# Performance work log

Hardware: AMD Instinct MI355X
Metric: run time of the kernel (lower is better)

## Reference

```python
import jax, jax.numpy as jnp
import numpy as np

B = 32768; E = 9; RANK = 50; K = 2
N_ENT = 40943; N_REL = 22
LOSS_COEF = 0.01; NOISE_EPS = 0.01
EPS = float(np.finfo(np.float64).eps)


def setup_inputs():
    key = jax.random.key(0)
    ks = jax.random.split(key, 12)
    q0 = jax.random.randint(ks[0], (B,), 0, N_ENT)
    q1 = jax.random.randint(ks[1], (B,), 0, N_REL)
    q2 = jax.random.randint(ks[2], (B,), 0, N_ENT)
    queries = jnp.stack([q0, q1, q2], axis=1)
    t2 = jax.random.randint(ks[3], (B,), 0, N_ENT)
    these_queries = jnp.stack([q0, q1, t2], axis=1)
    D = E * RANK
    entity = jax.random.normal(ks[4], (N_ENT, D), jnp.float32) / D
    rel = jax.random.normal(ks[5], (N_REL, 2 * D), jnp.float32) / (2 * D)
    rel_diag = 2.0 * jax.random.uniform(ks[6], (N_REL, D), jnp.float32) - 1.0
    bh = jnp.zeros((N_ENT, 1), jnp.float32)
    bt = jnp.zeros((N_ENT, 1), jnp.float32)
    c_param = jnp.ones((N_REL, 1), jnp.float32)
    cnn_w = 0.1 * jax.random.normal(ks[7], (1, 1, 5, 5), jnp.float32)
    cnn_b = jnp.zeros((1,), jnp.float32)
    h2e_w = 0.05 * jax.random.normal(ks[8], (E, 128), jnp.float32)
    h2e_b = jnp.zeros((E,), jnp.float32)
    cnnn_w = 0.1 * jax.random.normal(ks[9], (1, 1, 5, 5), jnp.float32)
    cnnn_b = jnp.zeros((1,), jnp.float32)
    h2en_w = 0.05 * jax.random.normal(ks[10], (E, 128), jnp.float32)
    h2en_b = jnp.zeros((E,), jnp.float32)
    noise = jax.random.normal(ks[11], (B, E), jnp.float32)
    return {"queries": queries, "these_queries": these_queries, "entity": entity,
            "rel": rel, "rel_diag": rel_diag, "bh": bh, "bt": bt, "c_param": c_param,
            "cnn_w": cnn_w, "cnn_b": cnn_b, "h2e_w": h2e_w, "h2e_b": h2e_b,
            "cnnn_w": cnnn_w, "cnnn_b": cnnn_b, "h2en_w": h2en_w, "h2en_b": h2en_b,
            "noise": noise}


def _conv(x, w, b):
    # x: [B,1,27,50], w: [1,1,5,5], stride 3, VALID -> [B,1,8,16]
    y = jax.lax.conv_general_dilated(x, w, (3, 3), 'VALID',
                                     dimension_numbers=('NCHW', 'OIHW', 'NCHW'))
    return y + b.reshape(1, -1, 1, 1)


def _phi(z):
    # standard normal CDF
    return 0.5 * (1.0 + jax.lax.erf(z * 0.7071067811865476))


def _givens_rot(r, x):
    # r, x: [B,E,RANK]; rotate consecutive dim-pairs by normalized (cos,sin) from r
    shp = r.shape[:-1] + (RANK // 2, 2)
    r2 = r.reshape(shp); x2 = x.reshape(shp)
    nrm = jnp.maximum(jnp.linalg.norm(r2, axis=-1, keepdims=True), 1e-15)
    cs = r2 / nrm
    o0 = cs[..., 0] * x2[..., 0] - cs[..., 1] * x2[..., 1]
    o1 = cs[..., 1] * x2[..., 0] + cs[..., 0] * x2[..., 1]
    return jnp.stack([o0, o1], axis=-1).reshape(r.shape)


def _cv_squared(v):
    return jnp.var(v, ddof=1) / (jnp.mean(v) ** 2 + 1e-10)


def reference(queries, these_queries, entity, rel, rel_diag, bh, bt, c_param,
              cnn_w, cnn_b, h2e_w, h2e_b, cnnn_w, cnnn_b, h2en_w, h2en_b, noise):
    q0, q1 = queries[:, 0], queries[:, 1]
    t2 = these_queries[:, 2]
    head = entity[q0]                  # [B, E*RANK]
    rel_q = rel[q1]                    # [B, 2*E*RANK]
    rel_diag_q = rel_diag[q1]          # [B, E*RANK]
    c = jax.nn.softplus(c_param[q1])   # [B, 1]
    lhs_b = bh[q0]                     # [B, 1]
    rhs_b = bt[t2]                     # [B, 1]
    rhs_e = entity[t2]                 # [B, E*RANK]

    # ---- noisy top-k gating ----
    x = jnp.concatenate([head, rel_q], axis=-1).reshape(-1, 1, 3 * E, RANK)
    feat = _conv(x, cnn_w, cnn_b).reshape(-1, 128)
    clean = feat @ h2e_w.T + h2e_b                      # [B, E]
    feat_n = _conv(x, cnnn_w, cnnn_b).reshape(-1, 128)
    raw_std = feat_n @ h2en_w.T + h2en_b
    std = jax.nn.softplus(raw_std) + NOISE_EPS
    noisy = clean + noise * std                         # train=1

    top_logits, top_idx = jax.lax.top_k(noisy, K + 1)
    tk_logits = top_logits[:, :K]
    tk_idx = top_idx[:, :K]
    tk_gates = jax.nn.softmax(tk_logits, axis=-1)
    gates = jnp.zeros_like(noisy).at[jnp.arange(noisy.shape[0])[:, None], tk_idx].set(tk_gates)

    thr_in = top_logits[:, K:K + 1]
    thr_out = top_logits[:, K - 1:K]
    is_in = noisy > thr_in
    prob = jnp.where(is_in, _phi((clean - thr_in) / std), _phi((clean - thr_out) / std))
    load = prob.sum(0)
    importance = gates.sum(0)
    loss = LOSS_COEF * (_cv_squared(importance) + _cv_squared(load))

    # ---- experts, computed densely over [B, E, RANK] then masked-combined ----
    head_r = head.reshape(-1, E, RANK)
    rhs_r = rhs_e.reshape(-1, E, RANK)
    rel_r = rel_q.reshape(-1, E, 2 * RANK)
    rd_r = rel_diag_q.reshape(-1, E, RANK)
    lhs = _givens_rot(rd_r, head_r) + rel_r[..., :RANK]
    dist2 = jnp.sum((lhs - rhs_r) ** 2, axis=-1)        # [B, E]
    score = lhs_b + rhs_b - c * dist2                   # [B, E]

    # SparseDispatcher.combine with use_log_sum_exp=True, multiply_by_gates=False
    mask = gates > 0
    s = jnp.sum(jnp.where(mask, jnp.exp(score), 0.0), axis=1, keepdims=True)
    y = jnp.log(jnp.where(s == 0, EPS, s))              # [B, 1]
    return y, loss
```

## Files before the change

kernel.cpp:

```cpp
#include <hip/hip_runtime.h>
#include <math.h>

#define BATCH 32768
#define NE 9
#define RANK 50
#define DIM 450
#define REL_DIM 900
#define N_REL 22
#define EPSV 2.2204460492503131e-16f

__device__ __forceinline__ float softplusf(float x) {
    return (x > 20.f) ? x : log1pf(expf(x));
}
__device__ __forceinline__ float phif(float z) {
    return 0.5f * (1.f + erff(z * 0.70710678118654752f));
}

__global__ __launch_bounds__(64) void k_pre(
    const float* __restrict__ rel, const float* __restrict__ rel_diag,
    const float* __restrict__ c_param,
    const float* __restrict__ cnn_w, const float* __restrict__ cnn_b,
    const float* __restrict__ cnnn_w, const float* __restrict__ cnnn_b,
    const float* __restrict__ h2e_w, const float* __restrict__ h2en_w,
    float* __restrict__ cs_tab, float* __restrict__ pre_out, float* __restrict__ c_soft)
{
    const int r = blockIdx.x;
    const int l = threadIdx.x;
    __shared__ float rl[REL_DIM];
    __shared__ float fA[80], fB[80];

    const float* relp = rel + (size_t)r * REL_DIM;
    for (int i = l; i < REL_DIM; i += 64) rl[i] = relp[i];
    __syncthreads();

    const float cb0 = cnn_b[0], cb1 = cnnn_b[0];
    for (int idx = l; idx < 80; idx += 64) {
        int o = 48 + idx;
        int oh = o >> 4, ow = o & 15;
        const float* base = rl + (oh * 3 - 9) * RANK + ow * 3;
        float a0 = cb0, a1 = cb1;
#pragma unroll
        for (int i = 0; i < 5; ++i)
#pragma unroll
            for (int j = 0; j < 5; ++j) {
                float v = base[i * RANK + j];
                a0 = fmaf(v, cnn_w[i * 5 + j], a0);
                a1 = fmaf(v, cnnn_w[i * 5 + j], a1);
            }
        fA[idx] = a0; fB[idx] = a1;
    }
    __syncthreads();

    if (l < 18) {
        int e = (l < 9) ? l : (l - 9);
        const float* w = ((l < 9) ? (h2e_w + e * 128) : (h2en_w + e * 128)) + 48;
        const float* f = (l < 9) ? fA : fB;
        float acc = 0.f;
#pragma unroll 8
        for (int t = 0; t < 80; ++t) acc = fmaf(f[t], w[t], acc);
        pre_out[r * 18 + l] = acc;
    }
    if (l == 63) c_soft[r] = softplusf(c_param[r]);

    const float2* rd2 = (const float2*)(rel_diag + (size_t)r * DIM);
    float2* cs2 = (float2*)(cs_tab + (size_t)r * DIM);
    for (int u = l; u < 225; u += 64) {
        float2 v = rd2[u];
        float nrm = fmaxf(sqrtf(v.x * v.x + v.y * v.y), 1e-15f);
        cs2[u] = make_float2(v.x / nrm, v.y / nrm);
    }
}

__global__ __launch_bounds__(64) void k_main(
    const int* __restrict__ queries, const int* __restrict__ these_queries,
    const float* __restrict__ entity, const float* __restrict__ rel,
    const float* __restrict__ bh, const float* __restrict__ bt,
    const float* __restrict__ cnn_w, const float* __restrict__ cnn_b,
    const float* __restrict__ h2e_w, const float* __restrict__ h2e_b,
    const float* __restrict__ cnnn_w, const float* __restrict__ cnnn_b,
    const float* __restrict__ h2en_w, const float* __restrict__ h2en_b,
    const float* __restrict__ noise,
    const float* __restrict__ cs_tab, const float* __restrict__ pre_out,
    const float* __restrict__ c_soft,
    float* __restrict__ y_out, float* __restrict__ ws_rows)
{
    const int b = blockIdx.x;
    const int l = threadIdx.x;

    __shared__ __align__(16) float xs[552];
    __shared__ __align__(16) float2 fs[51];
    __shared__ float clean_s[NE], stdv_s[NE], noisy_s[NE];
    __shared__ int   sidx[2];
    __shared__ float sg[2];
    __shared__ float sthr[2];

    const int q0 = queries[b * 3 + 0];
    const int q1 = queries[b * 3 + 1];
    const int t2 = these_queries[b * 3 + 2];

    const float2* hp2 = (const float2*)(entity + (size_t)q0 * DIM);
    const float2* rp2 = (const float2*)(rel + (size_t)q1 * REL_DIM);

    float2 h2[4];
#pragma unroll
    for (int k = 0; k < 4; ++k) { int i = l + 64 * k; if (i < 225) h2[k] = hp2[i]; }
    float2 rr2 = make_float2(0.f, 0.f);
    if (l < 50) rr2 = rp2[l];
    float nz = 0.f;
    if (l < NE) nz = noise[(size_t)b * NE + l];
    float pre_v = 0.f;
    if (l < 18) pre_v = pre_out[q1 * 18 + l];

    float2* xs2 = (float2*)xs;
#pragma unroll
    for (int k = 0; k < 4; ++k) { int i = l + 64 * k; if (i < 225) xs2[i] = h2[k]; }
    if (l < 50) xs2[225 + l] = rr2;
    __syncthreads();

    if (l < 48) {
        int oh = l >> 4, ow = l & 15;
        const float* base = xs + (oh * 3) * RANK + ow * 3;
        float a0 = cnn_b[0], a1 = cnnn_b[0];
#pragma unroll
        for (int i = 0; i < 5; ++i)
#pragma unroll
            for (int j = 0; j < 5; ++j) {
                float v = base[i * RANK + j];
                a0 = fmaf(v, cnn_w[i * 5 + j], a0);
                a1 = fmaf(v, cnnn_w[i * 5 + j], a1);
            }
        fs[l + (l >> 4)] = make_float2(a0, a1);
    }
    __syncthreads();

    float acc = 0.f;
    if (l < 54) {
        int chunk = l / 18, j = l - chunk * 18;
        int e = (j < 9) ? j : (j - 9);
        const float* wrow = ((j < 9) ? (h2e_w + e * 128) : (h2en_w + e * 128)) + chunk * 16;
        int fbase = chunk * 17;
        if (j < 9) {
#pragma unroll
            for (int k = 0; k < 16; ++k) acc = fmaf(fs[fbase + k].x, wrow[k], acc);
        } else {
#pragma unroll
            for (int k = 0; k < 16; ++k) acc = fmaf(fs[fbase + k].y, wrow[k], acc);
        }
    }
    float pA = __shfl_down(acc, 18);
    float pB = __shfl_down(acc, 36);
    float tot = acc + pA + pB;
    if (l < 9)        clean_s[l]     = tot + pre_v + h2e_b[l];
    else if (l < 18)  stdv_s[l - 9]  = softplusf(tot + pre_v + h2en_b[l - 9]) + 0.01f;
    __syncthreads();
    if (l < NE) noisy_s[l] = fmaf(nz, stdv_s[l], clean_s[l]);
    __syncthreads();

    if (l == 0) {
        int i0 = -1, i1 = -1;
        float v0 = -__builtin_huge_valf(), v1 = v0, v2 = v0;
#pragma unroll
        for (int e = 0; e < NE; ++e) {
            float v = noisy_s[e];
            if (v > v0)      { v2 = v1; v1 = v0; i1 = i0; v0 = v; i0 = e; }
            else if (v > v1) { v2 = v1; v1 = v; i1 = e; }
            else if (v > v2) { v2 = v; }
        }
        float e1 = expf(v1 - v0);
        float inv = 1.f / (1.f + e1);
        sidx[0] = i0; sidx[1] = i1;
        sg[0] = inv; sg[1] = e1 * inv;
        sthr[0] = v2; sthr[1] = v1;
    }
    __syncthreads();

    float contrib = 0.f;
    bool act = (l < 25) || (l >= 32 && l < 57);
    if (act) {
        int sel = (l >= 32) ? 1 : 0;
        int p = l - 32 * sel;
        int e = sidx[sel];
        int u = e * 25 + p;
        float2 cs = *(const float2*)(cs_tab + (size_t)q1 * DIM + 2 * u);
        float2 rl = *(const float2*)(rel + (size_t)q1 * REL_DIM + e * 100 + 2 * p);
        float2 rh = *(const float2*)(entity + (size_t)t2 * DIM + 2 * u);
        float2 x  = xs2[u];
        float o0 = cs.x * x.x - cs.y * x.y + rl.x;
        float o1 = cs.y * x.x + cs.x * x.y + rl.y;
        float d0 = o0 - rh.x, d1 = o1 - rh.y;
        contrib = fmaf(d0, d0, d1 * d1);
    }

    if (l < NE) {
        float g = (l == sidx[0]) ? sg[0] : ((l == sidx[1]) ? sg[1] : 0.f);
        ws_rows[(size_t)b * 18 + l] = g;
    } else if (l < 18) {
        int e = l - 9;
        float thr_in = sthr[0], thr_out = sthr[1];
        float n = noisy_s[e];
        float thr = (n > thr_in) ? thr_in : thr_out;
        ws_rows[(size_t)b * 18 + 9 + e] = phif((clean_s[e] - thr) / stdv_s[e]);
    }

#pragma unroll
    for (int off = 16; off; off >>= 1) contrib += __shfl_xor(contrib, off);
    float d2b = __shfl(contrib, 32);
    if (l == 0) {
        float c = c_soft[q1];
        float base = bh[q0] + bt[t2];
        float s = expf(base - c * contrib) + expf(base - c * d2b);
        y_out[b] = logf((s == 0.f) ? EPSV : s);
    }
}

__global__ __launch_bounds__(64) void k_reduce(const float* __restrict__ ws_rows,
                                               float* __restrict__ partials)
{
    const int blk = blockIdx.x, t = threadIdx.x;
    float acc[18];
#pragma unroll
    for (int j = 0; j < 18; ++j) acc[j] = 0.f;
    const int r0 = blk * 128 + t * 2;
#pragma unroll
    for (int rr = 0; rr < 2; ++rr) {
        const float2* row = (const float2*)(ws_rows + (size_t)(r0 + rr) * 18);
#pragma unroll
        for (int j = 0; j < 9; ++j) {
            float2 v = row[j];
            acc[2 * j] += v.x; acc[2 * j + 1] += v.y;
        }
    }
#pragma unroll
    for (int j = 0; j < 18; ++j) {
        float v = acc[j];
        for (int off = 32; off; off >>= 1) v += __shfl_down(v, off);
        if (t == 0) partials[blk * 18 + j] = v;
    }
}

__global__ __launch_bounds__(64) void k_loss(const float* __restrict__ partials,
                                             float* __restrict__ out)
{
    __shared__ float sums[18];
    const int t = threadIdx.x;
    if (t < 18) {
        float s = 0.f;
        for (int p = 0; p < 256; ++p) s += partials[p * 18 + t];
        sums[t] = s;
    }
    __syncthreads();
    if (t == 0) {
        float loss = 0.f;
#pragma unroll
        for (int part = 0; part < 2; ++part) {
            const float* v = sums + part * NE;
            float mean = 0.f;
            for (int i = 0; i < NE; ++i) mean += v[i];
            mean /= 9.f;
            float var = 0.f;
            for (int i = 0; i < NE; ++i) { float d = v[i] - mean; var += d * d; }
            var /= 8.f;
            loss += var / (mean * mean + 1e-10f);
        }
        out[BATCH] = 0.01f * loss;
    }
}

extern "C" void kernel_launch(void* const* d_in, const int* in_sizes, int n_in,
                              void* d_out, int out_size, void* d_ws, size_t ws_size,
                              hipStream_t stream)
{
    const int*   queries = (const int*)d_in[0];
    const int*   these   = (const int*)d_in[1];
    const float* entity  = (const float*)d_in[2];
    const float* rel     = (const float*)d_in[3];
    const float* rel_dg  = (const float*)d_in[4];
    const float* bh      = (const float*)d_in[5];
    const float* bt      = (const float*)d_in[6];
    const float* c_par   = (const float*)d_in[7];
    const float* cnn_w   = (const float*)d_in[8];
    const float* cnn_b   = (const float*)d_in[9];
    const float* h2e_w   = (const float*)d_in[10];
    const float* h2e_b   = (const float*)d_in[11];
    const float* cnnn_w  = (const float*)d_in[12];
    const float* cnnn_b  = (const float*)d_in[13];
    const float* h2en_w  = (const float*)d_in[14];
    const float* h2en_b  = (const float*)d_in[15];
    const float* noise   = (const float*)d_in[16];

    float* y  = (float*)d_out;
    float* ws = (float*)d_ws;
    float* ws_rows  = ws;
    float* partials = ws + (size_t)BATCH * 18;
    float* cs_tab   = partials + 256 * 18;
    float* pre_out  = cs_tab + N_REL * DIM;
    float* c_soft   = pre_out + N_REL * 18;

    k_pre<<<N_REL, 64, 0, stream>>>(rel, rel_dg, c_par, cnn_w, cnn_b, cnnn_w, cnnn_b,
                                    h2e_w, h2en_w, cs_tab, pre_out, c_soft);
    k_main<<<BATCH, 64, 0, stream>>>(queries, these, entity, rel, bh, bt,
                                     cnn_w, cnn_b, h2e_w, h2e_b, cnnn_w, cnnn_b,
                                     h2en_w, h2en_b, noise, cs_tab, pre_out, c_soft,
                                     y, ws_rows);
    k_reduce<<<256, 64, 0, stream>>>(ws_rows, partials);
    k_loss<<<1, 64, 0, stream>>>(partials, y);
}
```

Baseline: 187.4 us.

## Pack four batch rows per block and fuse loss into reduce via atomic counter

k_main now runs 256-thread blocks where each wavefront handles one batch row with its own shared-memory slice, cutting the block count by four. The goal is lower per-block scheduling overhead and higher occupancy. The separate single-block loss kernel is folded into k_reduce: a last-block-done atomic counter, reset in k_pre, lets the final block compute the loss, saving one launch. Block-wide __syncthreads now stall all four waves together, and the counter scheme depends on the reset being ordered before k_reduce.

```diff
diff --git a/kernel.cpp b/kernel.cpp
--- a/kernel.cpp
+++ b/kernel.cpp
@@ -22,7 +22,8 @@
     const float* __restrict__ cnn_w, const float* __restrict__ cnn_b,
     const float* __restrict__ cnnn_w, const float* __restrict__ cnnn_b,
     const float* __restrict__ h2e_w, const float* __restrict__ h2en_w,
-    float* __restrict__ cs_tab, float* __restrict__ pre_out, float* __restrict__ c_soft)
+    float* __restrict__ cs_tab, float* __restrict__ pre_out, float* __restrict__ c_soft,
+    int* __restrict__ counter)
 {
     const int r = blockIdx.x;
     const int l = threadIdx.x;
@@ -61,6 +62,7 @@
         pre_out[r * 18 + l] = acc;
     }
     if (l == 63) c_soft[r] = softplusf(c_param[r]);
+    if (r == 0 && l == 62) *counter = 0;
 
     const float2* rd2 = (const float2*)(rel_diag + (size_t)r * DIM);
     float2* cs2 = (float2*)(cs_tab + (size_t)r * DIM);
@@ -71,7 +73,16 @@
     }
 }
 
-__global__ __launch_bounds__(64) void k_main(
+struct WaveShm {
+    float  xs[552];
+    float2 fs[51];
+    float  clean[NE], stdv[NE], noisy[NE];
+    float  sg[2], sthr[2];
+    int    sidx[2];
+    int    pad;
+};
+
+__global__ __launch_bounds__(256, 8) void k_main(
     const int* __restrict__ queries, const int* __restrict__ these_queries,
     const float* __restrict__ entity, const float* __restrict__ rel,
     const float* __restrict__ bh, const float* __restrict__ bt,
@@ -84,15 +95,11 @@
     const float* __restrict__ c_soft,
     float* __restrict__ y_out, float* __restrict__ ws_rows)
 {
-    const int b = blockIdx.x;
-    const int l = threadIdx.x;
-
-    __shared__ __align__(16) float xs[552];
-    __shared__ __align__(16) float2 fs[51];
-    __shared__ float clean_s[NE], stdv_s[NE], noisy_s[NE];
-    __shared__ int   sidx[2];
-    __shared__ float sg[2];
-    __shared__ float sthr[2];
+    __shared__ WaveShm shm[4];
+    const int w = threadIdx.x >> 6;
+    const int l = threadIdx.x & 63;
+    const int b = blockIdx.x * 4 + w;
+    WaveShm& S = shm[w];
 
     const int q0 = queries[b * 3 + 0];
     const int q1 = queries[b * 3 + 1];
@@ -111,7 +118,7 @@
     float pre_v = 0.f;
     if (l < 18) pre_v = pre_out[q1 * 18 + l];
 
-    float2* xs2 = (float2*)xs;
+    float2* xs2 = (float2*)S.xs;
 #pragma unroll
     for (int k = 0; k < 4; ++k) { int i = l + 64 * k; if (i < 225) xs2[i] = h2[k]; }
     if (l < 50) xs2[225 + l] = rr2;
@@ -119,7 +126,7 @@
 
     if (l < 48) {
         int oh = l >> 4, ow = l & 15;
-        const float* base = xs + (oh * 3) * RANK + ow * 3;
+        const float* base = S.xs + (oh * 3) * RANK + ow * 3;
         float a0 = cnn_b[0], a1 = cnnn_b[0];
 #pragma unroll
         for (int i = 0; i < 5; ++i)
@@ -129,7 +136,7 @@
                 a0 = fmaf(v, cnn_w[i * 5 + j], a0);
                 a1 = fmaf(v, cnnn_w[i * 5 + j], a1);
             }
-        fs[l + (l >> 4)] = make_float2(a0, a1);
+        S.fs[l + (l >> 4)] = make_float2(a0, a1);
     }
     __syncthreads();
 
@@ -141,19 +148,19 @@
         int fbase = chunk * 17;
         if (j < 9) {
 #pragma unroll
-            for (int k = 0; k < 16; ++k) acc = fmaf(fs[fbase + k].x, wrow[k], acc);
+            for (int k = 0; k < 16; ++k) acc = fmaf(S.fs[fbase + k].x, wrow[k], acc);
         } else {
 #pragma unroll
-            for (int k = 0; k < 16; ++k) acc = fmaf(fs[fbase + k].y, wrow[k], acc);
+            for (int k = 0; k < 16; ++k) acc = fmaf(S.fs[fbase + k].y, wrow[k], acc);
         }
     }
     float pA = __shfl_down(acc, 18);
     float pB = __shfl_down(acc, 36);
     float tot = acc + pA + pB;
-    if (l < 9)        clean_s[l]     = tot + pre_v + h2e_b[l];
-    else if (l < 18)  stdv_s[l - 9]  = softplusf(tot + pre_v + h2en_b[l - 9]) + 0.01f;
-    __syncthreads();
-    if (l < NE) noisy_s[l] = fmaf(nz, stdv_s[l], clean_s[l]);
+    if (l < 9)        S.clean[l]     = tot + pre_v + h2e_b[l];
+    else if (l < 18)  S.stdv[l - 9]  = softplusf(tot + pre_v + h2en_b[l - 9]) + 0.01f;
+    __syncthreads();
+    if (l < NE) S.noisy[l] = fmaf(nz, S.stdv[l], S.clean[l]);
     __syncthreads();
 
     if (l == 0) {
@@ -161,16 +168,16 @@
         float v0 = -__builtin_huge_valf(), v1 = v0, v2 = v0;
 #pragma unroll
         for (int e = 0; e < NE; ++e) {
-            float v = noisy_s[e];
+            float v = S.noisy[e];
             if (v > v0)      { v2 = v1; v1 = v0; i1 = i0; v0 = v; i0 = e; }
             else if (v > v1) { v2 = v1; v1 = v; i1 = e; }
             else if (v > v2) { v2 = v; }
         }
         float e1 = expf(v1 - v0);
         float inv = 1.f / (1.f + e1);
-        sidx[0] = i0; sidx[1] = i1;
-        sg[0] = inv; sg[1] = e1 * inv;
-        sthr[0] = v2; sthr[1] = v1;
+        S.sidx[0] = i0; S.sidx[1] = i1;
+        S.sg[0] = inv; S.sg[1] = e1 * inv;
+        S.sthr[0] = v2; S.sthr[1] = v1;
     }
     __syncthreads();
 
@@ -179,7 +186,7 @@
     if (act) {
         int sel = (l >= 32) ? 1 : 0;
         int p = l - 32 * sel;
-        int e = sidx[sel];
+        int e = S.sidx[sel];
         int u = e * 25 + p;
         float2 cs = *(const float2*)(cs_tab + (size_t)q1 * DIM + 2 * u);
         float2 rl = *(const float2*)(rel + (size_t)q1 * REL_DIM + e * 100 + 2 * p);
@@ -192,14 +199,14 @@
     }
 
     if (l < NE) {
-        float g = (l == sidx[0]) ? sg[0] : ((l == sidx[1]) ? sg[1] : 0.f);
+        float g = (l == S.sidx[0]) ? S.sg[0] : ((l == S.sidx[1]) ? S.sg[1] : 0.f);
         ws_rows[(size_t)b * 18 + l] = g;
     } else if (l < 18) {
         int e = l - 9;
-        float thr_in = sthr[0], thr_out = sthr[1];
-        float n = noisy_s[e];
+        float thr_in = S.sthr[0], thr_out = S.sthr[1];
+        float n = S.noisy[e];
         float thr = (n > thr_in) ? thr_in : thr_out;
-        ws_rows[(size_t)b * 18 + 9 + e] = phif((clean_s[e] - thr) / stdv_s[e]);
+        ws_rows[(size_t)b * 18 + 9 + e] = phif((S.clean[e] - thr) / S.stdv[e]);
     }
 
 #pragma unroll
@@ -214,7 +221,9 @@
 }
 
 __global__ __launch_bounds__(64) void k_reduce(const float* __restrict__ ws_rows,
-                                               float* __restrict__ partials)
+                                               float* __restrict__ partials,
+                                               int* __restrict__ counter,
+                                               float* __restrict__ out)
 {
     const int blk = blockIdx.x, t = threadIdx.x;
     float acc[18];
@@ -236,13 +245,18 @@
         for (int off = 32; off; off >>= 1) v += __shfl_down(v, off);
         if (t == 0) partials[blk * 18 + j] = v;
     }
-}
-
-__global__ __launch_bounds__(64) void k_loss(const float* __restrict__ partials,
-                                             float* __restrict__ out)
-{
+
+    __shared__ int is_last;
+    __threadfence();
+    if (t == 0) {
+        int old = atomicAdd(counter, 1);
+        is_last = (old == 255) ? 1 : 0;
+    }
+    __syncthreads();
+    if (!is_last) return;
+    __threadfence();
+
     __shared__ float sums[18];
-    const int t = threadIdx.x;
     if (t < 18) {
         float s = 0.f;
         for (int p = 0; p < 256; ++p) s += partials[p * 18 + t];
@@ -295,13 +309,13 @@
     float* cs_tab   = partials + 256 * 18;
     float* pre_out  = cs_tab + N_REL * DIM;
     float* c_soft   = pre_out + N_REL * 18;
+    int*   counter  = (int*)(c_soft + N_REL);
 
     k_pre<<<N_REL, 64, 0, stream>>>(rel, rel_dg, c_par, cnn_w, cnn_b, cnnn_w, cnnn_b,
-                                    h2e_w, h2en_w, cs_tab, pre_out, c_soft);
-    k_main<<<BATCH, 64, 0, stream>>>(queries, these, entity, rel, bh, bt,
-                                     cnn_w, cnn_b, h2e_w, h2e_b, cnnn_w, cnnn_b,
-                                     h2en_w, h2en_b, noise, cs_tab, pre_out, c_soft,
-                                     y, ws_rows);
-    k_reduce<<<256, 64, 0, stream>>>(ws_rows, partials);
-    k_loss<<<1, 64, 0, stream>>>(partials, y);
-}
+                                    h2e_w, h2en_w, cs_tab, pre_out, c_soft, counter);
+    k_main<<<BATCH / 4, 256, 0, stream>>>(queries, these, entity, rel, bh, bt,
+                                          cnn_w, cnn_b, h2e_w, h2e_b, cnnn_w, cnnn_b,
+                                          h2en_w, h2en_b, noise, cs_tab, pre_out, c_soft,
+                                          y, ws_rows);
+    k_reduce<<<256, 64, 0, stream>>>(ws_rows, partials, counter, y);
+}
```

Measured after the change: 199.5 us. 1.06x slower.
